# Performance work log

Hardware: AMD Instinct MI355X
Metric: run time of the kernel (lower is better)

The kernel has to match this reference:

```python
import jax, jax.numpy as jnp
import numpy as np

B, LQ, LKV, D, H, LOOKBACK = 4, 4096, 512, 512, 8, 8
DH = D // H
SCALE = DH ** -0.5


def setup_inputs() -> dict:
    key = jax.random.key(0)
    ks = jax.random.split(key, 12)
    q = jax.random.normal(ks[0], (B, LQ, D), dtype=jnp.float32)
    kv_src = jax.random.normal(ks[1], (B, LKV, D), dtype=jnp.float32)
    seg_id = jnp.sort(jax.random.randint(ks[2], (B, LQ), 0, LKV), axis=-1)
    kv_mask = jnp.zeros((B, LKV), dtype=bool)
    q_pad_mask = jnp.zeros((B, LQ), dtype=bool)
    s = D ** -0.5
    Wq = jax.random.normal(ks[3], (D, D), jnp.float32) * s
    bq = jnp.zeros((D,), jnp.float32)
    Wk = jax.random.normal(ks[4], (D, D), jnp.float32) * s
    bk = jnp.zeros((D,), jnp.float32)
    Wv = jax.random.normal(ks[5], (D, D), jnp.float32) * s
    bv = jnp.zeros((D,), jnp.float32)
    Wo = jax.random.normal(ks[6], (D, D), jnp.float32) * s
    bo = jnp.zeros((D,), jnp.float32)
    return {"q": q, "kv_src": kv_src, "seg_id": seg_id, "kv_mask": kv_mask,
            "q_pad_mask": q_pad_mask, "Wq": Wq, "bq": bq, "Wk": Wk, "bk": bk,
            "Wv": Wv, "bv": bv, "Wo": Wo, "bo": bo}


def _split_heads(x):
    b, l, _ = x.shape
    return x.reshape(b, l, H, DH).transpose(0, 2, 1, 3)  # (B,H,L,Dh)


def reference(q, kv_src, seg_id, kv_mask, q_pad_mask, Wq, bq, Wk, bk, Wv, bv, Wo, bo):
    qh = _split_heads(q @ Wq + bq)        # (B,H,Lq,Dh)
    kh = _split_heads(kv_src @ Wk + bk)   # (B,H,Lkv,Dh)
    vh = _split_heads(kv_src @ Wv + bv)   # (B,H,Lkv,Dh)

    offsets = jnp.arange(LOOKBACK + 1)
    gather = jnp.clip(seg_id[:, :, None] - offsets, 0, LKV - 1)  # (B,Lq,Kw)

    # per-batch windowed gather of K/V: (B,H,Lq,Kw,Dh)
    k_sel = jax.vmap(lambda kb, gb: kb[:, gb])(kh, gather)
    v_sel = jax.vmap(lambda vb, gb: vb[:, gb])(vh, gather)

    scores = jnp.einsum('bhld,bhlkd->bhlk', qh, k_sel) * SCALE
    mask_sel = jax.vmap(lambda m, g: m[g])(kv_mask, gather)  # (B,Lq,Kw)
    scores = jnp.where(mask_sel[:, None], jnp.finfo(scores.dtype).min, scores)
    probs = jax.nn.softmax(scores, axis=-1)

    out = jnp.einsum('bhlk,bhlkd->bhld', probs, v_sel)
    out = out.transpose(0, 2, 1, 3).reshape(q.shape[0], q.shape[1], D)
    out = out @ Wo + bo
    out = jnp.where(q_pad_mask[:, :, None], 0.0, out)
    return out
```

## Files before the change

kernel.cpp:

```cpp
#include <hip/hip_runtime.h>
#include <hip/hip_bf16.h>
#include <float.h>

typedef unsigned short u16;
typedef unsigned long long u64;
typedef __attribute__((ext_vector_type(8))) short short8;
typedef __attribute__((ext_vector_type(4))) float f32x4;

#define NB       4
#define LQ       4096
#define LKV      512
#define DMODEL   512
#define NH       8
#define DH       64
#define KW       9
#define SCALE    0.125f

#define BM 64
#define BN 64
#define BK 64

__device__ inline float bf2f(u16 v) { return __uint_as_float(((unsigned)v) << 16); }
__device__ inline unsigned pk2(float a, float b) {
    unsigned r;
    asm("v_cvt_pk_bf16_f32 %0, %1, %2" : "=v"(r) : "v"(a), "v"(b));
    return r;
}
__device__ inline u16 f2bf(float f) {
    unsigned u = __float_as_uint(f);
    return (u16)((u + 0x7fffu + ((u >> 16) & 1u)) >> 16);
}
__device__ inline void gload16(const u16* g, u16* l) {
    __builtin_amdgcn_global_load_lds((const __attribute__((address_space(1))) void*)g,
                                     (__attribute__((address_space(3))) void*)l, 16, 0, 0);
}
__device__ inline short8 cvt8(const float4 v0, const float4 v1) {
    union { unsigned u[4]; short8 s; } r;
    r.u[0] = pk2(v0.x, v0.y);
    r.u[1] = pk2(v0.z, v0.w);
    r.u[2] = pk2(v1.x, v1.y);
    r.u[3] = pk2(v1.z, v1.w);
    return r.s;
}
__device__ inline int xcd_swz(int id, int nwg) {
    const int cpx = nwg >> 3;
    return (id & 7) * cpx + (id >> 3);
}

__global__ __launch_bounds__(256) void transpose4_kernel(
    const float* __restrict__ Wq, const float* __restrict__ Wk,
    const float* __restrict__ Wv, const float* __restrict__ Wo,
    u16* __restrict__ Wqt, u16* __restrict__ Wkvt, u16* __restrict__ Wot)
{
    __shared__ float tile[32][33];
    const int z = blockIdx.z;
    const float* src = (z == 0) ? Wq : (z == 1) ? Wk : (z == 2) ? Wv : Wo;
    u16* dst = (z == 0) ? Wqt : (z == 3) ? Wot : Wkvt;
    const int roff = (z == 2) ? DMODEL : 0;

    const int tx = threadIdx.x & 31, ty = threadIdx.x >> 5;
    const int x0 = blockIdx.x * 32, y0 = blockIdx.y * 32;
    #pragma unroll
    for (int i = 0; i < 4; ++i)
        tile[ty + i * 8][tx] = src[(y0 + ty + i * 8) * DMODEL + x0 + tx];
    __syncthreads();
    #pragma unroll
    for (int i = 0; i < 4; ++i)
        dst[(long long)(roff + x0 + ty + i * 8) * DMODEL + y0 + tx] = f2bf(tile[tx][ty + i * 8]);
}

template<int A_F32, int OUT_F32, int PACK_MASK>
__global__ __launch_bounds__(256, 8) void gemm64_kernel(
    const void* __restrict__ Ain, const u16* __restrict__ Bt,
    const float* __restrict__ bias0, const float* __restrict__ bias1, int nsplit,
    void* __restrict__ Cout, int N, int K, int cshift,
    const unsigned char* __restrict__ row_mask,
    const unsigned char* __restrict__ kv_mask_in, u64* __restrict__ mbits_out)
{
    __shared__ u16 As[BM * BK];
    __shared__ u16 Bs[BN * BK];

    const int tid = threadIdx.x;
    const int w = tid >> 6, l = tid & 63;
    const int wr = w >> 1, wc = w & 1;

    if (PACK_MASK) {
        if (blockIdx.x == 0 && tid < 36) {
            if (tid < 32) {
                const int b = tid >> 3, wd = tid & 7;
                const unsigned char* p = kv_mask_in + b * LKV + wd * 64;
                u64 m = 0;
                for (int i = 0; i < 64; ++i) m |= ((u64)(p[i] != 0)) << i;
                mbits_out[b * 9 + wd] = m;
            } else {
                mbits_out[(tid - 32) * 9 + 8] = 0ULL;
            }
        }
    }

    const int wg = xcd_swz((int)blockIdx.x, (int)gridDim.x);
    const int bx = wg & ((1 << cshift) - 1);
    const int by = wg >> cshift;
    const int brow = by * BM, bcol = bx * BN;

    const int srow   = l >> 3;
    const int schunk = ((l & 7) ^ srow) * 8;
    const long long ar0 = brow + w * 16 + srow;
    const long long br0 = bcol + w * 16 + srow;
    const u16*   gA0  = (const u16*)Ain   + ar0 * K + schunk;
    const u16*   gA1  = gA0 + 8 * K;
    const float* gAf0 = (const float*)Ain + ar0 * K + schunk;
    const float* gAf1 = gAf0 + 8 * K;
    const u16* gB0 = Bt + br0 * K + schunk;
    const u16* gB1 = gB0 + 8 * K;
    u16* lA0 = As + (w * 16) * BK;
    u16* lA1 = As + (w * 16 + 8) * BK;
    u16* lB0 = Bs + (w * 16) * BK;
    u16* lB1 = Bs + (w * 16 + 8) * BK;

    const int hi = l >> 4, lr = l & 15;
    const int r7 = lr & 7;

    f32x4 acc[2][2] = {};

    float4 p0, p1, p2, p3;
    if (A_F32) {
        p0 = *(const float4*)(gAf0);     p1 = *(const float4*)(gAf0 + 4);
        p2 = *(const float4*)(gAf1);     p3 = *(const float4*)(gAf1 + 4);
    }

    for (int k0 = 0; k0 < K; k0 += BK) {
        if (A_F32) {
            *(short8*)(lA0 + l * 8) = cvt8(p0, p1);
            *(short8*)(lA1 + l * 8) = cvt8(p2, p3);
        } else {
            gload16(gA0 + k0, lA0);
            gload16(gA1 + k0, lA1);
        }
        gload16(gB0 + k0, lB0);
        gload16(gB1 + k0, lB1);
        __syncthreads();

        if (A_F32 && k0 + BK < K) {
            p0 = *(const float4*)(gAf0 + k0 + BK); p1 = *(const float4*)(gAf0 + k0 + BK + 4);
            p2 = *(const float4*)(gAf1 + k0 + BK); p3 = *(const float4*)(gAf1 + k0 + BK + 4);
        }

        #pragma unroll
        for (int g2 = 0; g2 < 2; ++g2) {
            const int slot = ((g2 * 4 + hi) ^ r7) * 8;
            short8 a[2], b[2];
            #pragma unroll
            for (int m = 0; m < 2; ++m)
                a[m] = *(const short8*)&As[(wr * 32 + m * 16 + lr) * BK + slot];
            #pragma unroll
            for (int n = 0; n < 2; ++n)
                b[n] = *(const short8*)&Bs[(wc * 32 + n * 16 + lr) * BK + slot];
            #pragma unroll
            for (int m = 0; m < 2; ++m)
                #pragma unroll
                for (int n = 0; n < 2; ++n)
                    acc[m][n] = __builtin_amdgcn_mfma_f32_16x16x32_bf16(a[m], b[n], acc[m][n], 0, 0, 0);
        }
        __syncthreads();
    }

    #pragma unroll
    for (int m = 0; m < 2; ++m) {
        #pragma unroll
        for (int n = 0; n < 2; ++n) {
            const int col = bcol + wc * 32 + n * 16 + lr;
            const float bv = (col < nsplit) ? bias0[col] : bias1[col - nsplit];
            const int row0 = brow + wr * 32 + m * 16 + hi * 4;
            if (OUT_F32) {
                #pragma unroll
                for (int r = 0; r < 4; ++r) {
                    const int row = row0 + r;
                    const float v = acc[m][n][r] + bv;
                    ((float*)Cout)[(long long)row * N + col] =
                        (row_mask != nullptr && row_mask[row]) ? 0.0f : v;
                }
            } else {
                const unsigned pa = pk2(acc[m][n][0] + bv, acc[m][n][1] + bv);
                const unsigned pb = pk2(acc[m][n][2] + bv, acc[m][n][3] + bv);
                u16* cp = (u16*)Cout + (long long)row0 * N + col;
                cp[0]           = (u16)pa;
                cp[(long long)N]     = (u16)(pa >> 16);
                cp[(long long)2 * N] = (u16)pb;
                cp[(long long)3 * N] = (u16)(pb >> 16);
            }
        }
    }
}

__global__ __launch_bounds__(256, 4) void qproj_attn_kernel(
    const float* __restrict__ Aq, const u16* __restrict__ Bt,
    const float* __restrict__ bias, const u16* __restrict__ khv,
    const int* __restrict__ seg_id, const u64* __restrict__ mbits,
    u16* __restrict__ atb)
{
    __shared__ u16 smem[BM * BK + BN * BK];
    u16* As = smem;
    u16* Bs = smem + BM * BK;
    u16* qt = smem;

    const int tid = threadIdx.x;
    const int w = tid >> 6, l = tid & 63;
    const int wr = w >> 1, wc = w & 1;

    const int wg = xcd_swz((int)blockIdx.x, (int)gridDim.x);
    const int bx = wg & 7;
    const int by = wg >> 3;
    const int brow = by * BM, bcol = bx * BN;
    const int K = DMODEL;
    const int head = bx;

    const int srow   = l >> 3;
    const int schunk = ((l & 7) ^ srow) * 8;
    const long long ar0 = brow + w * 16 + srow;
    const long long br0 = bcol + w * 16 + srow;
    const float* gAf0 = Aq + ar0 * K + schunk;
    const float* gAf1 = gAf0 + 8 * K;
    const u16* gB0 = Bt + br0 * K + schunk;
    const u16* gB1 = gB0 + 8 * K;
    u16* lA0 = As + (w * 16) * BK;
    u16* lA1 = As + (w * 16 + 8) * BK;
    u16* lB0 = Bs + (w * 16) * BK;
    u16* lB1 = Bs + (w * 16 + 8) * BK;

    const int hi = l >> 4, lr = l & 15;
    const int r7 = lr & 7;

    f32x4 acc[2][2] = {};

    float4 p0 = *(const float4*)(gAf0), p1 = *(const float4*)(gAf0 + 4);
    float4 p2 = *(const float4*)(gAf1), p3 = *(const float4*)(gAf1 + 4);

    for (int k0 = 0; k0 < K; k0 += BK) {
        *(short8*)(lA0 + l * 8) = cvt8(p0, p1);
        *(short8*)(lA1 + l * 8) = cvt8(p2, p3);
        gload16(gB0 + k0, lB0);
        gload16(gB1 + k0, lB1);
        __syncthreads();

        if (k0 + BK < K) {
            p0 = *(const float4*)(gAf0 + k0 + BK); p1 = *(const float4*)(gAf0 + k0 + BK + 4);
            p2 = *(const float4*)(gAf1 + k0 + BK); p3 = *(const float4*)(gAf1 + k0 + BK + 4);
        }

        #pragma unroll
        for (int g2 = 0; g2 < 2; ++g2) {
            const int slot = ((g2 * 4 + hi) ^ r7) * 8;
            short8 a[2], b[2];
            #pragma unroll
            for (int m = 0; m < 2; ++m)
                a[m] = *(const short8*)&As[(wr * 32 + m * 16 + lr) * BK + slot];
            #pragma unroll
            for (int n = 0; n < 2; ++n)
                b[n] = *(const short8*)&Bs[(wc * 32 + n * 16 + lr) * BK + slot];
            #pragma unroll
            for (int m = 0; m < 2; ++m)
                #pragma unroll
                for (int n = 0; n < 2; ++n)
                    acc[m][n] = __builtin_amdgcn_mfma_f32_16x16x32_bf16(a[m], b[n], acc[m][n], 0, 0, 0);
        }
        __syncthreads();
    }

    #pragma unroll
    for (int m = 0; m < 2; ++m) {
        #pragma unroll
        for (int n = 0; n < 2; ++n) {
            const int col = wc * 32 + n * 16 + lr;
            const float bv = bias[bcol + col];
            const int row0 = wr * 32 + m * 16 + hi * 4;
            const unsigned pa = pk2(acc[m][n][0] + bv, acc[m][n][1] + bv);
            const unsigned pb = pk2(acc[m][n][2] + bv, acc[m][n][3] + bv);
            const int cslot = (col & 7);
            qt[(row0 + 0) * BN + (((col >> 3) ^ ((row0 + 0) & 7)) << 3) + cslot] = (u16)pa;
            qt[(row0 + 1) * BN + (((col >> 3) ^ ((row0 + 1) & 7)) << 3) + cslot] = (u16)(pa >> 16);
            qt[(row0 + 2) * BN + (((col >> 3) ^ ((row0 + 2) & 7)) << 3) + cslot] = (u16)pb;
            qt[(row0 + 3) * BN + (((col >> 3) ^ ((row0 + 3) & 7)) << 3) + cslot] = (u16)(pb >> 16);
        }
    }
    __syncthreads();

    const int dchunk = tid & 7;
    #pragma unroll
    for (int p = 0; p < 2; ++p) {
        const int row = p * 32 + (tid >> 3);
        const long long bl = brow + row;
        const int b = (int)(bl >> 12);
        const int seg = seg_id[bl];
        const u16* kvb = khv + (long long)b * LKV * 1024;

        int lo = seg - (KW - 1); if (lo < 0) lo = 0;
        const int w0 = lo >> 6, off = lo & 63;
        const u64* mb = mbits + b * 9;
        u64 wv = mb[w0] >> off;
        if (off) wv |= mb[w0 + 1] << (64 - off);

        const short8 q8 = *(const short8*)&qt[row * BN + ((dchunk ^ (row & 7)) << 3)];
        float qf[8];
        #pragma unroll
        for (int e = 0; e < 8; ++e) qf[e] = bf2f((u16)q8[e]);

        int idxs[KW];
        #pragma unroll
        for (int j = 0; j < KW; ++j) {
            int idx = seg - j; if (idx < 0) idx = 0;
            idxs[j] = idx;
        }

        short8 k8[KW];
        #pragma unroll
        for (int j = 0; j < KW; ++j)
            k8[j] = *(const short8*)&kvb[(long long)idxs[j] * 1024 + head * DH + dchunk * 8];

        float d[KW];
        #pragma unroll
        for (int j = 0; j < KW; ++j) {
            float d0 = 0.0f, d1 = 0.0f;
            #pragma unroll
            for (int e = 0; e < 8; e += 2) {
                d0 = fmaf(qf[e],     bf2f((u16)k8[j][e]),     d0);
                d1 = fmaf(qf[e + 1], bf2f((u16)k8[j][e + 1]), d1);
            }
            d[j] = d0 + d1;
        }
        #pragma unroll
        for (int j = 0; j < KW; ++j) d[j] += __shfl_xor(d[j], 1);
        #pragma unroll
        for (int j = 0; j < KW; ++j) d[j] += __shfl_xor(d[j], 2);
        #pragma unroll
        for (int j = 0; j < KW; ++j) d[j] += __shfl_xor(d[j], 4);

        float sc[KW];
        #pragma unroll
        for (int j = 0; j < KW; ++j) {
            float s = d[j] * SCALE;
            if ((wv >> (idxs[j] - lo)) & 1) s = -FLT_MAX;
            sc[j] = s;
        }

        short8 v8[KW];
        #pragma unroll
        for (int j = 0; j < KW; ++j)
            v8[j] = *(const short8*)&kvb[(long long)idxs[j] * 1024 + DMODEL + head * DH + dchunk * 8];

        float mx = sc[0];
        #pragma unroll
        for (int j = 1; j < KW; ++j) mx = fmaxf(mx, sc[j]);
        float den = 0.0f;
        #pragma unroll
        for (int j = 0; j < KW; ++j) { sc[j] = __expf(sc[j] - mx); den += sc[j]; }
        const float inv = 1.0f / den;

        float o[8];
        #pragma unroll
        for (int e = 0; e < 8; ++e) o[e] = 0.0f;
        #pragma unroll
        for (int j = 0; j < KW; ++j) {
            const float pj = sc[j];
            #pragma unroll
            for (int e = 0; e < 8; ++e)
                o[e] = fmaf(pj, bf2f((u16)v8[j][e]), o[e]);
        }

        union { unsigned u[4]; short8 s; } ov;
        #pragma unroll
        for (int e = 0; e < 4; ++e)
            ov.u[e] = pk2(o[2 * e] * inv, o[2 * e + 1] * inv);
        *(short8*)&atb[bl * DMODEL + head * DH + dchunk * 8] = ov.s;
    }
}

extern "C" void kernel_launch(void* const* d_in, const int* in_sizes, int n_in,
                              void* d_out, int out_size, void* d_ws, size_t ws_size,
                              hipStream_t stream) {
    const float*         q          = (const float*)d_in[0];
    const float*         kv_src     = (const float*)d_in[1];
    const int*           seg_id     = (const int*)d_in[2];
    const unsigned char* kv_mask    = (const unsigned char*)d_in[3];
    const unsigned char* q_pad_mask = (const unsigned char*)d_in[4];
    const float*         Wq         = (const float*)d_in[5];
    const float*         bq         = (const float*)d_in[6];
    const float*         Wk         = (const float*)d_in[7];
    const float*         bk         = (const float*)d_in[8];
    const float*         Wv         = (const float*)d_in[9];
    const float*         bv         = (const float*)d_in[10];
    const float*         Wo         = (const float*)d_in[11];
    const float*         bo         = (const float*)d_in[12];
    float* out = (float*)d_out;

    const long long MQ  = (long long)NB * LQ;
    const long long MKV = (long long)NB * LKV;

    char* wsb = (char*)d_ws;
    u16* Wqt  = (u16*)wsb;  wsb += DMODEL * DMODEL * 2;
    u16* Wkvt = (u16*)wsb;  wsb += 2 * DMODEL * DMODEL * 2;
    u16* Wot  = (u16*)wsb;  wsb += DMODEL * DMODEL * 2;
    u16* khv  = (u16*)wsb;  wsb += MKV * 2 * DMODEL * 2;
    u16* atb  = (u16*)wsb;  wsb += MQ  * DMODEL * 2;
    u64* mbits = (u64*)wsb; wsb += NB * 9 * 8;

    dim3 blk(256);

    transpose4_kernel<<<dim3(DMODEL / 32, DMODEL / 32, 4), blk, 0, stream>>>(
        Wq, Wk, Wv, Wo, Wqt, Wkvt, Wot);

    gemm64_kernel<1, 0, 1><<<dim3((unsigned)((2 * DMODEL / BN) * (MKV / BM))), blk, 0, stream>>>(
        kv_src, Wkvt, bk, bv, DMODEL, khv, 2 * DMODEL, DMODEL, 4, nullptr, kv_mask, mbits);

    qproj_attn_kernel<<<dim3((unsigned)((DMODEL / BN) * (MQ / BM))), blk, 0, stream>>>(
        q, Wqt, bq, khv, seg_id, mbits, atb);

    gemm64_kernel<0, 1, 0><<<dim3((unsigned)((DMODEL / BN) * (MQ / BM))), blk, 0, stream>>>(
        atb, Wot, bo, bo, DMODEL, out, DMODEL, DMODEL, 3, q_pad_mask, nullptr, nullptr);
}
```

Baseline: 71.56 us.

## Split fused Q-projection+attention kernel into separate GEMM and attention kernels

Measured after the change: 76.15 us. +6.4%, slower.

```diff
diff --git a/kernel.cpp b/kernel.cpp
--- a/kernel.cpp
+++ b/kernel.cpp
@@ -193,186 +193,99 @@
     }
 }
 
-__global__ __launch_bounds__(256, 4) void qproj_attn_kernel(
-    const float* __restrict__ Aq, const u16* __restrict__ Bt,
-    const float* __restrict__ bias, const u16* __restrict__ khv,
+__global__ __launch_bounds__(256, 4) void attn_kernel(
+    const u16* __restrict__ qh, const u16* __restrict__ khv,
     const int* __restrict__ seg_id, const u64* __restrict__ mbits,
     u16* __restrict__ atb)
 {
-    __shared__ u16 smem[BM * BK + BN * BK];
-    u16* As = smem;
-    u16* Bs = smem + BM * BK;
-    u16* qt = smem;
-
     const int tid = threadIdx.x;
-    const int w = tid >> 6, l = tid & 63;
-    const int wr = w >> 1, wc = w & 1;
-
     const int wg = xcd_swz((int)blockIdx.x, (int)gridDim.x);
-    const int bx = wg & 7;
-    const int by = wg >> 3;
-    const int brow = by * BM, bcol = bx * BN;
-    const int K = DMODEL;
-    const int head = bx;
-
-    const int srow   = l >> 3;
-    const int schunk = ((l & 7) ^ srow) * 8;
-    const long long ar0 = brow + w * 16 + srow;
-    const long long br0 = bcol + w * 16 + srow;
-    const float* gAf0 = Aq + ar0 * K + schunk;
-    const float* gAf1 = gAf0 + 8 * K;
-    const u16* gB0 = Bt + br0 * K + schunk;
-    const u16* gB1 = gB0 + 8 * K;
-    u16* lA0 = As + (w * 16) * BK;
-    u16* lA1 = As + (w * 16 + 8) * BK;
-    u16* lB0 = Bs + (w * 16) * BK;
-    u16* lB1 = Bs + (w * 16 + 8) * BK;
-
-    const int hi = l >> 4, lr = l & 15;
-    const int r7 = lr & 7;
-
-    f32x4 acc[2][2] = {};
-
-    float4 p0 = *(const float4*)(gAf0), p1 = *(const float4*)(gAf0 + 4);
-    float4 p2 = *(const float4*)(gAf1), p3 = *(const float4*)(gAf1 + 4);
-
-    for (int k0 = 0; k0 < K; k0 += BK) {
-        *(short8*)(lA0 + l * 8) = cvt8(p0, p1);
-        *(short8*)(lA1 + l * 8) = cvt8(p2, p3);
-        gload16(gB0 + k0, lB0);
-        gload16(gB1 + k0, lB1);
-        __syncthreads();
-
-        if (k0 + BK < K) {
-            p0 = *(const float4*)(gAf0 + k0 + BK); p1 = *(const float4*)(gAf0 + k0 + BK + 4);
-            p2 = *(const float4*)(gAf1 + k0 + BK); p3 = *(const float4*)(gAf1 + k0 + BK + 4);
-        }
-
+    const long long item = (long long)wg * 32 + (tid >> 3);
+    const int dchunk = tid & 7;
+    const int head = (int)(item & 7);
+    const long long bl = item >> 3;
+    const int b = (int)(bl >> 12);
+    const int seg = seg_id[bl];
+    const u16* kvb = khv + (long long)b * LKV * 1024;
+
+    int lo = seg - (KW - 1); if (lo < 0) lo = 0;
+    const int w0 = lo >> 6, off = lo & 63;
+    const u64* mb = mbits + b * 9;
+    u64 wv = mb[w0] >> off;
+    if (off) wv |= mb[w0 + 1] << (64 - off);
+
+    const short8 q8 = *(const short8*)&qh[bl * DMODEL + head * DH + dchunk * 8];
+    float qf[8];
+    #pragma unroll
+    for (int e = 0; e < 8; ++e) qf[e] = bf2f((u16)q8[e]);
+
+    int idxs[KW];
+    #pragma unroll
+    for (int j = 0; j < KW; ++j) {
+        int idx = seg - j; if (idx < 0) idx = 0;
+        idxs[j] = idx;
+    }
+
+    short8 k8[KW];
+    #pragma unroll
+    for (int j = 0; j < KW; ++j)
+        k8[j] = *(const short8*)&kvb[(long long)idxs[j] * 1024 + head * DH + dchunk * 8];
+
+    float d[KW];
+    #pragma unroll
+    for (int j = 0; j < KW; ++j) {
+        float d0 = 0.0f, d1 = 0.0f;
         #pragma unroll
-        for (int g2 = 0; g2 < 2; ++g2) {
-            const int slot = ((g2 * 4 + hi) ^ r7) * 8;
-            short8 a[2], b[2];
-            #pragma unroll
-            for (int m = 0; m < 2; ++m)
-                a[m] = *(const short8*)&As[(wr * 32 + m * 16 + lr) * BK + slot];
-            #pragma unroll
-            for (int n = 0; n < 2; ++n)
-                b[n] = *(const short8*)&Bs[(wc * 32 + n * 16 + lr) * BK + slot];
-            #pragma unroll
-            for (int m = 0; m < 2; ++m)
-                #pragma unroll
-                for (int n = 0; n < 2; ++n)
-                    acc[m][n] = __builtin_amdgcn_mfma_f32_16x16x32_bf16(a[m], b[n], acc[m][n], 0, 0, 0);
-        }
-        __syncthreads();
-    }
-
-    #pragma unroll
-    for (int m = 0; m < 2; ++m) {
+        for (int e = 0; e < 8; e += 2) {
+            d0 = fmaf(qf[e],     bf2f((u16)k8[j][e]),     d0);
+            d1 = fmaf(qf[e + 1], bf2f((u16)k8[j][e + 1]), d1);
+        }
+        d[j] = d0 + d1;
+    }
+    #pragma unroll
+    for (int j = 0; j < KW; ++j) d[j] += __shfl_xor(d[j], 1);
+    #pragma unroll
+    for (int j = 0; j < KW; ++j) d[j] += __shfl_xor(d[j], 2);
+    #pragma unroll
+    for (int j = 0; j < KW; ++j) d[j] += __shfl_xor(d[j], 4);
+
+    float sc[KW];
+    #pragma unroll
+    for (int j = 0; j < KW; ++j) {
+        float s = d[j] * SCALE;
+        if ((wv >> (idxs[j] - lo)) & 1) s = -FLT_MAX;
+        sc[j] = s;
+    }
+
+    short8 v8[KW];
+    #pragma unroll
+    for (int j = 0; j < KW; ++j)
+        v8[j] = *(const short8*)&kvb[(long long)idxs[j] * 1024 + DMODEL + head * DH + dchunk * 8];
+
+    float mx = sc[0];
+    #pragma unroll
+    for (int j = 1; j < KW; ++j) mx = fmaxf(mx, sc[j]);
+    float den = 0.0f;
+    #pragma unroll
+    for (int j = 0; j < KW; ++j) { sc[j] = __expf(sc[j] - mx); den += sc[j]; }
+    const float inv = 1.0f / den;
+
+    float o[8];
+    #pragma unroll
+    for (int e = 0; e < 8; ++e) o[e] = 0.0f;
+    #pragma unroll
+    for (int j = 0; j < KW; ++j) {
+        const float pj = sc[j];
         #pragma unroll
-        for (int n = 0; n < 2; ++n) {
-            const int col = wc * 32 + n * 16 + lr;
-            const float bv = bias[bcol + col];
-            const int row0 = wr * 32 + m * 16 + hi * 4;
-            const unsigned pa = pk2(acc[m][n][0] + bv, acc[m][n][1] + bv);
-            const unsigned pb = pk2(acc[m][n][2] + bv, acc[m][n][3] + bv);
-            const int cslot = (col & 7);
-            qt[(row0 + 0) * BN + (((col >> 3) ^ ((row0 + 0) & 7)) << 3) + cslot] = (u16)pa;
-            qt[(row0 + 1) * BN + (((col >> 3) ^ ((row0 + 1) & 7)) << 3) + cslot] = (u16)(pa >> 16);
-            qt[(row0 + 2) * BN + (((col >> 3) ^ ((row0 + 2) & 7)) << 3) + cslot] = (u16)pb;
-            qt[(row0 + 3) * BN + (((col >> 3) ^ ((row0 + 3) & 7)) << 3) + cslot] = (u16)(pb >> 16);
-        }
-    }
-    __syncthreads();
-
-    const int dchunk = tid & 7;
-    #pragma unroll
-    for (int p = 0; p < 2; ++p) {
-        const int row = p * 32 + (tid >> 3);
-        const long long bl = brow + row;
-        const int b = (int)(bl >> 12);
-        const int seg = seg_id[bl];
-        const u16* kvb = khv + (long long)b * LKV * 1024;
-
-        int lo = seg - (KW - 1); if (lo < 0) lo = 0;
-        const int w0 = lo >> 6, off = lo & 63;
-        const u64* mb = mbits + b * 9;
-        u64 wv = mb[w0] >> off;
-        if (off) wv |= mb[w0 + 1] << (64 - off);
-
-        const short8 q8 = *(const short8*)&qt[row * BN + ((dchunk ^ (row & 7)) << 3)];
-        float qf[8];
-        #pragma unroll
-        for (int e = 0; e < 8; ++e) qf[e] = bf2f((u16)q8[e]);
-
-        int idxs[KW];
-        #pragma unroll
-        for (int j = 0; j < KW; ++j) {
-            int idx = seg - j; if (idx < 0) idx = 0;
-            idxs[j] = idx;
-        }
-
-        short8 k8[KW];
-        #pragma unroll
-        for (int j = 0; j < KW; ++j)
-            k8[j] = *(const short8*)&kvb[(long long)idxs[j] * 1024 + head * DH + dchunk * 8];
-
-        float d[KW];
-        #pragma unroll
-        for (int j = 0; j < KW; ++j) {
-            float d0 = 0.0f, d1 = 0.0f;
-            #pragma unroll
-            for (int e = 0; e < 8; e += 2) {
-                d0 = fmaf(qf[e],     bf2f((u16)k8[j][e]),     d0);
-                d1 = fmaf(qf[e + 1], bf2f((u16)k8[j][e + 1]), d1);
-            }
-            d[j] = d0 + d1;
-        }
-        #pragma unroll
-        for (int j = 0; j < KW; ++j) d[j] += __shfl_xor(d[j], 1);
-        #pragma unroll
-        for (int j = 0; j < KW; ++j) d[j] += __shfl_xor(d[j], 2);
-        #pragma unroll
-        for (int j = 0; j < KW; ++j) d[j] += __shfl_xor(d[j], 4);
-
-        float sc[KW];
-        #pragma unroll
-        for (int j = 0; j < KW; ++j) {
-            float s = d[j] * SCALE;
-            if ((wv >> (idxs[j] - lo)) & 1) s = -FLT_MAX;
-            sc[j] = s;
-        }
-
-        short8 v8[KW];
-        #pragma unroll
-        for (int j = 0; j < KW; ++j)
-            v8[j] = *(const short8*)&kvb[(long long)idxs[j] * 1024 + DMODEL + head * DH + dchunk * 8];
-
-        float mx = sc[0];
-        #pragma unroll
-        for (int j = 1; j < KW; ++j) mx = fmaxf(mx, sc[j]);
-        float den = 0.0f;
-        #pragma unroll
-        for (int j = 0; j < KW; ++j) { sc[j] = __expf(sc[j] - mx); den += sc[j]; }
-        const float inv = 1.0f / den;
-
-        float o[8];
-        #pragma unroll
-        for (int e = 0; e < 8; ++e) o[e] = 0.0f;
-        #pragma unroll
-        for (int j = 0; j < KW; ++j) {
-            const float pj = sc[j];
-            #pragma unroll
-            for (int e = 0; e < 8; ++e)
-                o[e] = fmaf(pj, bf2f((u16)v8[j][e]), o[e]);
-        }
-
-        union { unsigned u[4]; short8 s; } ov;
-        #pragma unroll
-        for (int e = 0; e < 4; ++e)
-            ov.u[e] = pk2(o[2 * e] * inv, o[2 * e + 1] * inv);
-        *(short8*)&atb[bl * DMODEL + head * DH + dchunk * 8] = ov.s;
-    }
+        for (int e = 0; e < 8; ++e)
+            o[e] = fmaf(pj, bf2f((u16)v8[j][e]), o[e]);
+    }
+
+    union { unsigned u[4]; short8 s; } ov;
+    #pragma unroll
+    for (int e = 0; e < 4; ++e)
+        ov.u[e] = pk2(o[2 * e] * inv, o[2 * e + 1] * inv);
+    *(short8*)&atb[bl * DMODEL + head * DH + dchunk * 8] = ov.s;
 }
 
 extern "C" void kernel_launch(void* const* d_in, const int* in_sizes, int n_in,
@@ -401,6 +314,7 @@
     u16* Wkvt = (u16*)wsb;  wsb += 2 * DMODEL * DMODEL * 2;
     u16* Wot  = (u16*)wsb;  wsb += DMODEL * DMODEL * 2;
     u16* khv  = (u16*)wsb;  wsb += MKV * 2 * DMODEL * 2;
+    u16* qh   = (u16*)wsb;  wsb += MQ  * DMODEL * 2;
     u16* atb  = (u16*)wsb;  wsb += MQ  * DMODEL * 2;
     u64* mbits = (u64*)wsb; wsb += NB * 9 * 8;
 
@@ -412,8 +326,11 @@
     gemm64_kernel<1, 0, 1><<<dim3((unsigned)((2 * DMODEL / BN) * (MKV / BM))), blk, 0, stream>>>(
         kv_src, Wkvt, bk, bv, DMODEL, khv, 2 * DMODEL, DMODEL, 4, nullptr, kv_mask, mbits);
 
-    qproj_attn_kernel<<<dim3((unsigned)((DMODEL / BN) * (MQ / BM))), blk, 0, stream>>>(
-        q, Wqt, bq, khv, seg_id, mbits, atb);
+    gemm64_kernel<1, 0, 0><<<dim3((unsigned)((DMODEL / BN) * (MQ / BM))), blk, 0, stream>>>(
+        q, Wqt, bq, bq, DMODEL, qh, DMODEL, DMODEL, 3, nullptr, nullptr, nullptr);
+
+    attn_kernel<<<dim3((unsigned)(MQ * NH / 32)), blk, 0, stream>>>(
+        qh, khv, seg_id, mbits, atb);
 
     gemm64_kernel<0, 1, 0><<<dim3((unsigned)((DMODEL / BN) * (MQ / BM))), blk, 0, stream>>>(
         atb, Wot, bo, bo, DMODEL, out, DMODEL, DMODEL, 3, q_pad_mask, nullptr, nullptr);
```
